# Kernel tuning notes

Measured on AMD Instinct MI355X. Metric: run time of the kernel, lower is better.

## Reference

```python
import jax, jax.numpy as jnp
import numpy as np

NUM_KP = 17
EDGES = [(0,1),(1,3),(0,2),(2,4),(0,5),(5,7),(7,9),(5,11),(11,13),(13,15),(0,6),(6,8),(8,10),(6,12),(12,14),(14,16)]
NUM_EDGES = len(EDGES)
IMG_H = IMG_W = 401


def bilinear_sampler(x, v):
    # x, v: [N, H, W, 2]. Faithful port of the TF gather_nd bilinear sampler
    # (pad-by-1 border, floor/ceil corners, out-of-bounds -> index 0 into pad).
    N, H, W, C = x.shape
    xp = jnp.pad(x, ((0, 0), (1, 1), (1, 1), (0, 0)))  # zeros pad
    vx = v[..., 0]
    vy = v[..., 1]
    hgrid = jnp.arange(1, H + 1, dtype=jnp.float32)[None, :, None]  # [1,H,1]
    wgrid = jnp.arange(1, W + 1, dtype=jnp.float32)[None, None, :]  # [1,1,W]
    vx0 = jnp.floor(vx); vy0 = jnp.floor(vy)
    vx1 = jnp.ceil(vx);  vy1 = jnp.ceil(vy)
    iy0 = vy0 + hgrid; iy1 = vy1 + hgrid
    ix0 = vx0 + wgrid; ix1 = vx1 + wgrid
    Hf = jnp.float32(H); Wf = jnp.float32(W)
    mask = (ix0 < 1.0) | (iy0 < 1.0) | (ix1 > Wf) | (iy1 > Hf)
    zero = jnp.zeros_like(iy0)
    iy0 = jnp.where(mask, zero, iy0)
    iy1 = jnp.where(mask, zero, iy1)
    ix0 = jnp.where(mask, zero, ix0)
    ix1 = jnp.where(mask, zero, ix1)
    n = jnp.arange(N)[:, None, None]
    iy0i = iy0.astype(jnp.int32); iy1i = iy1.astype(jnp.int32)
    ix0i = ix0.astype(jnp.int32); ix1i = ix1.astype(jnp.int32)
    x00 = xp[n, iy0i, ix0i]  # [N,H,W,C]
    x01 = xp[n, iy1i, ix0i]
    x10 = xp[n, iy0i, ix1i]
    x11 = xp[n, iy1i, ix1i]
    dx = (vx - vx0)[..., None]
    dy = (vy - vy0)[..., None]
    w00 = (1.0 - dx) * (1.0 - dy)
    w01 = (1.0 - dx) * dy
    w10 = dx * (1.0 - dy)
    w11 = dx * dy
    return w00 * x00 + w01 * x01 + w10 * x10 + w11 * x11


def refine(base, offsets, num_steps=2):
    for _ in range(num_steps):
        base = base + bilinear_sampler(offsets, base)
    return base


def conv1x1(x, w, b):
    return jnp.einsum('nhwc,co->nhwo', x, w) + b


def resize(m):
    N, _, _, C = m.shape
    return jax.image.resize(m, (N, IMG_H, IMG_W, C), method='bilinear')


def setup_inputs() -> dict:
    key = jax.random.key(0)
    ks = jax.random.split(key, 11)
    N, H, W, Cin = 2, 13, 13, 2048
    s = 0.01
    return {
        'x': jax.random.normal(ks[0], (N, H, W, Cin), jnp.float32),
        'kp_w': jax.random.normal(ks[1], (Cin, NUM_KP), jnp.float32) * s,
        'kp_b': jax.random.normal(ks[2], (NUM_KP,), jnp.float32) * s,
        'so_w': jax.random.normal(ks[3], (Cin, 2 * NUM_KP), jnp.float32) * s,
        'so_b': jax.random.normal(ks[4], (2 * NUM_KP,), jnp.float32) * s,
        'mo_w': jax.random.normal(ks[5], (Cin, 4 * NUM_EDGES), jnp.float32) * s,
        'mo_b': jax.random.normal(ks[6], (4 * NUM_EDGES,), jnp.float32) * s,
        'lo_w': jax.random.normal(ks[7], (Cin, 2 * NUM_KP), jnp.float32) * s,
        'lo_b': jax.random.normal(ks[8], (2 * NUM_KP,), jnp.float32) * s,
        'ss_w': jax.random.normal(ks[9], (Cin, 1), jnp.float32) * s,
        'ss_b': jax.random.normal(ks[10], (1,), jnp.float32) * s,
    }


def reference(x, kp_w, kp_b, so_w, so_b, mo_w, mo_b, lo_w, lo_b, ss_w, ss_b):
    N = x.shape[0]
    kp = jax.nn.sigmoid(conv1x1(x, kp_w, kp_b))
    so = conv1x1(x, so_w, so_b)
    mo = conv1x1(x, mo_w, mo_b)
    lo = conv1x1(x, lo_w, lo_b)
    ss = jax.nn.sigmoid(conv1x1(x, ss_w, ss_b))
    kp, so, mo, lo, ss = (resize(m) for m in (kp, so, mo, lo, ss))
    # Split channels into (x,y)-offset groups: [K, N, H, W, 2]
    S = so.reshape(N, IMG_H, IMG_W, NUM_KP, 2).transpose(3, 0, 1, 2, 4)
    L = lo.reshape(N, IMG_H, IMG_W, NUM_KP, 2).transpose(3, 0, 1, 2, 4)
    # long: refine against itself, then against short offsets (2 steps each)
    Lr = jax.vmap(lambda l, s: refine(refine(l, l), s))(L, S)
    long_out = Lr.transpose(1, 2, 3, 0, 4).reshape(N, IMG_H, IMG_W, 2 * NUM_KP)
    # mid: one group per directed edge, refined against the target kp short offsets
    n_mid = 2 * NUM_EDGES
    M = mo.reshape(N, IMG_H, IMG_W, n_mid, 2).transpose(3, 0, 1, 2, 4)
    to_kp = jnp.array([e[1] for e in EDGES] + [e[0] for e in EDGES], dtype=jnp.int32)
    Mr = jax.vmap(lambda m, s: refine(m, s))(M, S[to_kp])
    mid_out = Mr.transpose(1, 2, 3, 0, 4).reshape(N, IMG_H, IMG_W, 4 * NUM_EDGES)
    return (kp, so, mid_out, long_out, ss)
```

## Files before the change

### kernel.cpp

```cpp
#include <hip/hip_runtime.h>
#include <math.h>

#define IMG 401
#define NKP 17
#define NMID 32
#define CCH 150

#define OFF_KP   0ULL
#define OFF_SO   5467234ULL
#define OFF_MID  16401702ULL
#define OFF_LONG 36984230ULL
#define OFF_SS   47918698ULL

#define SCc (13.0f/401.0f)
#define C0c (13.0f/802.0f - 0.5f)
#define ROWS 8

typedef float v2f __attribute__((ext_vector_type(2)));

__device__ float  g_coarse[2 * 169 * CCH];
__device__ float2 g_pairs[2 * 66 * 169];

__constant__ int TO_KP_C[32] = {1,3,2,4,5,7,9,11,13,15,6,8,10,12,14,16,
                                0,1,0,2,0,5,7,5,11,13,0,6,8,6,12,14};

__device__ __forceinline__ float med3(float a, float b, float c) {
  return __builtin_amdgcn_fmed3f(a, b, c);
}
__device__ __forceinline__ void store2(float* p, float a, float b) {
  *reinterpret_cast<float2*>(p) = make_float2(a, b);
}
__device__ __forceinline__ v2f ldb(const float2* p, int byteoff) {
  return *reinterpret_cast<const v2f*>(reinterpret_cast<const char*>(p) + byteoff);
}

__global__ __launch_bounds__(512)
void heads_kernel(const float* __restrict__ x,
                  const float* __restrict__ kp_w, const float* __restrict__ kp_b,
                  const float* __restrict__ so_w, const float* __restrict__ so_b,
                  const float* __restrict__ mo_w, const float* __restrict__ mo_b,
                  const float* __restrict__ lo_w, const float* __restrict__ lo_b,
                  const float* __restrict__ ss_w, const float* __restrict__ ss_b) {
  __shared__ float xs[2][2048];
  __shared__ float ps[2][300];
  const int p0 = blockIdx.x * 2;
  const int tid = threadIdx.x;
  const float* xr = x + (size_t)p0 * 2048;
  for (int t = tid; t < 4096; t += 512) xs[t >> 11][t & 2047] = xr[t];
  __syncthreads();
  const int part = tid / 150;
  const int c = tid - part * 150;
  float a0 = 0.f, a1 = 0.f;
  const float* bptr = nullptr; int cc = 0; bool sig = false;
  if (part < 3) {
    const float* wptr; int Ch;
    if (c < 17)       { wptr = kp_w; bptr = kp_b; Ch = 17; cc = c;       sig = true; }
    else if (c < 51)  { wptr = so_w; bptr = so_b; Ch = 34; cc = c - 17; }
    else if (c < 115) { wptr = mo_w; bptr = mo_b; Ch = 64; cc = c - 51; }
    else if (c < 149) { wptr = lo_w; bptr = lo_b; Ch = 34; cc = c - 115; }
    else              { wptr = ss_w; bptr = ss_b; Ch = 1;  cc = 0;       sig = true; }
    const float* wp = wptr + cc;
    const int k0 = part * 683, k1 = (part == 2) ? 2048 : (k0 + 683);
    #pragma unroll 8
    for (int k = k0; k < k1; ++k) {
      float wv = wp[k * Ch];
      a0 = fmaf(xs[0][k], wv, a0);
      a1 = fmaf(xs[1][k], wv, a1);
    }
    if (part) { ps[0][c + (part - 1) * 150] = a0; ps[1][c + (part - 1) * 150] = a1; }
  }
  __syncthreads();
  if (part == 0) {
    float b = bptr[cc];
    float v0 = a0 + ps[0][c] + ps[0][c + 150] + b;
    float v1 = a1 + ps[1][c] + ps[1][c + 150] + b;
    if (sig) { v0 = 1.0f / (1.0f + expf(-v0)); v1 = 1.0f / (1.0f + expf(-v1)); }
    g_coarse[(size_t)p0 * CCH + c] = v0;
    g_coarse[(size_t)(p0 + 1) * CCH + c] = v1;
    if (c >= 17 && c < 149) {
      int rel = c - 17;
      int fi = rel >> 1, lo = rel & 1;
      int nn0 = p0 / 169, pp0 = p0 - nn0 * 169;
      int nn1 = (p0 + 1) / 169, pp1 = (p0 + 1) - nn1 * 169;
      ((float*)g_pairs)[(((size_t)nn0 * 66 + fi) * 169 + pp0) * 2 + lo] = v0;
      ((float*)g_pairs)[(((size_t)nn1 * 66 + fi) * 169 + pp1) * 2 + lo] = v1;
    }
  }
}

struct Pix {
  v2f Q0, Q1, SWH, LOV, HIV;
  int ob;
  int pix;
  bool valid;
};

__device__ __forceinline__ Pix mkpix(int n, int w, int h) {
  Pix P;
  P.valid = (w < IMG) && (h < IMG);
  v2f WH = {(float)w, (float)h};
  v2f S = WH * SCc + C0c;
  float cx = med3(floorf(S.x), 0.f, 11.f);
  float cy = med3(floorf(S.y), 0.f, 11.f);
  float fx = med3(S.x - cx, 0.f, 1.f);
  float fy = med3(S.y - cy, 0.f, 1.f);
  float gx = 1.f - fx, gy = 1.f - fy;
  P.Q0 = (v2f){gx, fx} * gy;
  P.Q1 = (v2f){gx, fx} * fy;
  P.ob = (int)fmaf(cy, 104.f, cx * 8.f);
  P.SWH = S;
  P.LOV = -WH;
  P.HIV = 400.f - WH;
  P.pix = (n * IMG + h) * IMG + w;
  return P;
}

__device__ __forceinline__ v2f blp4b(const float2* __restrict__ F, const Pix& P) {
  return P.Q0.x * ldb(F, P.ob)       + P.Q0.y * ldb(F, P.ob + 8)
       + P.Q1.x * ldb(F, P.ob + 104) + P.Q1.y * ldb(F, P.ob + 112);
}

__device__ __forceinline__ v2f samplePk(const float2* __restrict__ F, v2f v, const Pix& P) {
  v2f F0 = {floorf(v.x), floorf(v.y)};
  v2f D  = v - F0;
  v2f E  = {D.x > 0.f ? 1.f : 0.f, D.y > 0.f ? 1.f : 0.f};
  v2f J1 = F0 + E;
  float sel = (F0.x < P.LOV.x || F0.y < P.LOV.y ||
               J1.x > P.HIV.x || J1.y > P.HIV.y) ? 0.f : 1.f;
  v2f S0 = F0 * SCc + P.SWH;
  v2f S1 = E  * SCc + S0;
  v2f C0 = {med3(floorf(S0.x), 0.f, 11.f), med3(floorf(S0.y), 0.f, 11.f)};
  v2f C1 = {med3(floorf(S1.x), 0.f, 11.f), med3(floorf(S1.y), 0.f, 11.f)};
  v2f U0t = S0 - C0;
  v2f U0 = {med3(U0t.x, 0.f, 1.f), med3(U0t.y, 0.f, 1.f)};
  v2f U1t = S1 - C1;
  v2f U1 = {med3(U1t.x, 0.f, 1.f), med3(U1t.y, 0.f, 1.f)};
  v2f DD = C1 - C0;
  v2f G  = 1.f - D;
  v2f E0 = G * U0;
  v2f E1 = D * U1;
  v2f Fd = D - E1;
  v2f M  = Fd - Fd * DD;
  v2f W0 = (G - E0) + M;
  v2f Tt = Fd - E1;
  v2f W1 = (E0 + E1) + Tt * DD;
  v2f W2 = E1 * DD;
  int a = (int)fmaf(C0.y, 104.f, C0.x * 8.f);
  v2f r0 = W0.x*ldb(F,a)     + W1.x*ldb(F,a+8)   + W2.x*ldb(F,a+16);
  v2f r1 = W0.x*ldb(F,a+104) + W1.x*ldb(F,a+112) + W2.x*ldb(F,a+120);
  v2f r2 = W0.x*ldb(F,a+208) + W1.x*ldb(F,a+216) + W2.x*ldb(F,a+224);
  v2f acc = W0.y*r0 + W1.y*r1 + W2.y*r2;
  return acc * sel;
}

__global__ __launch_bounds__(512, 6)
void refine512_kernel(float* __restrict__ out) {
  __shared__ float2 Sf[NKP * 169 + 14];
  __shared__ float2 Lf[NKP * 169 + 14];
  const int n = blockIdx.z;
  const int tid = threadIdx.x;
  const int w0 = blockIdx.x * 32, h0 = blockIdx.y * ROWS;

  {
    const float2* gS = g_pairs + (size_t)n * 66 * 169;
    const float2* gL = g_pairs + ((size_t)n * 66 + 49) * 169;
    for (int t = tid; t < NKP * 169; t += 512) { Sf[t] = gS[t]; Lf[t] = gL[t]; }
    if (tid < 14) {
      Sf[NKP * 169 + tid] = make_float2(0.f, 0.f);
      Lf[NKP * 169 + tid] = make_float2(0.f, 0.f);
    }
  }
  __syncthreads();

  const float* cb = g_coarse + (size_t)n * 169 * CCH;

  #pragma unroll 1
  for (int it = 0; it < 9; ++it) {
    int f = it * 512 + tid;
    if (f >= ROWS * 544) break;
    int r = f / 544, rem = f - r * 544;
    int px = rem / 17, c = rem - px * 17;
    Pix P = mkpix(n, w0 + px, h0 + r);
    if (P.valid) {
      const float* b0 = cb + (P.ob >> 3) * CCH + c;
      out[OFF_KP + (size_t)P.pix * 17 + c] =
          P.Q0.x*b0[0] + P.Q0.y*b0[CCH] + P.Q1.x*b0[13*CCH] + P.Q1.y*b0[14*CCH];
    }
  }

  if (tid < ROWS * 32) {
    int r = tid >> 5, px = tid & 31;
    Pix P = mkpix(n, w0 + px, h0 + r);
    if (P.valid) {
      const float* b0 = cb + (P.ob >> 3) * CCH + 149;
      out[OFF_SS + (size_t)P.pix] =
          P.Q0.x*b0[0] + P.Q0.y*b0[CCH] + P.Q1.x*b0[13*CCH] + P.Q1.y*b0[14*CCH];
    }
  }

  #pragma unroll 1
  for (int it = 0; it < 9; ++it) {
    int f = it * 512 + tid;
    if (f >= ROWS * 544) break;
    int r = f / 544, rem = f - r * 544;
    int px = rem / 17, k = rem - px * 17;
    Pix P = mkpix(n, w0 + px, h0 + r);
    const float2* S = Sf + k * 169;
    const float2* L = Lf + k * 169;
    v2f sv = blp4b(S, P);
    v2f b  = blp4b(L, P);
    b += samplePk(L, b, P);
    b += samplePk(L, b, P);
    b += samplePk(S, b, P);
    b += samplePk(S, b, P);
    if (P.valid) {
      store2(out + OFF_SO   + (size_t)P.pix * 34 + 2 * k, sv.x, sv.y);
      store2(out + OFF_LONG + (size_t)P.pix * 34 + 2 * k, b.x, b.y);
    }
  }

  const float2* gmo = g_pairs + ((size_t)n * 66 + 17) * 169;
  #pragma unroll 1
  for (int it = 0; it < 16; ++it) {
    int f = it * 512 + tid;
    int r = f >> 10, rem = f & 1023;
    int px = rem >> 5, g = rem & 31;
    Pix P = mkpix(n, w0 + px, h0 + r);
    v2f b = blp4b(gmo + g * 169, P);
    const float2* S = Sf + TO_KP_C[g] * 169;
    b += samplePk(S, b, P);
    b += samplePk(S, b, P);
    if (P.valid) store2(out + OFF_MID + (size_t)P.pix * 64 + 2 * g, b.x, b.y);
  }
}

extern "C" void kernel_launch(void* const* d_in, const int* in_sizes, int n_in,
                              void* d_out, int out_size, void* d_ws, size_t ws_size,
                              hipStream_t stream) {
  const float* x    = (const float*)d_in[0];
  const float* kp_w = (const float*)d_in[1];
  const float* kp_b = (const float*)d_in[2];
  const float* so_w = (const float*)d_in[3];
  const float* so_b = (const float*)d_in[4];
  const float* mo_w = (const float*)d_in[5];
  const float* mo_b = (const float*)d_in[6];
  const float* lo_w = (const float*)d_in[7];
  const float* lo_b = (const float*)d_in[8];
  const float* ss_w = (const float*)d_in[9];
  const float* ss_b = (const float*)d_in[10];
  float* out = (float*)d_out;

  heads_kernel<<<dim3(169), dim3(512), 0, stream>>>(x, kp_w, kp_b, so_w, so_b,
                                                    mo_w, mo_b, lo_w, lo_b,
                                                    ss_w, ss_b);
  refine512_kernel<<<dim3(13, 51, 2), dim3(512), 0, stream>>>(out);
}
```

Baseline: 161.6 us.

## Pad short-offset planes with clamped border to drop per-sample clamping

Stores the short-offset coarse planes in shared memory as 15x15 planes padded with replicated (edge-clamped) border values. A new sampler for those planes can then skip the med3 clamps on coarse indices and fractions, computing the cell step from a comparison instead of a second floor. The long planes keep the old unpadded layout. This cuts ALU work in the hot refinement samplers, in exchange for slightly more shared memory and a more complex staging loop with integer divides.

```diff
diff --git a/kernel.cpp b/kernel.cpp
--- a/kernel.cpp
+++ b/kernel.cpp
@@ -15,6 +15,9 @@
 #define SCc (13.0f/401.0f)
 #define C0c (13.0f/802.0f - 0.5f)
 #define ROWS 8
+#define PSTR 120
+#define PPL  225
+#define LBASE (17 * PPL)
 
 typedef float v2f __attribute__((ext_vector_type(2)));
 
@@ -91,6 +94,7 @@
 struct Pix {
   v2f Q0, Q1, SWH, LOV, HIV;
   int ob;
+  int obp;
   int pix;
   bool valid;
 };
@@ -107,7 +111,8 @@
   float gx = 1.f - fx, gy = 1.f - fy;
   P.Q0 = (v2f){gx, fx} * gy;
   P.Q1 = (v2f){gx, fx} * fy;
-  P.ob = (int)fmaf(cy, 104.f, cx * 8.f);
+  P.ob  = (int)fmaf(cy, 104.f, cx * 8.f);
+  P.obp = (int)fmaf(cy, (float)PSTR, cx * 8.f) + (PSTR + 8);
   P.SWH = S;
   P.LOV = -WH;
   P.HIV = 400.f - WH;
@@ -115,12 +120,16 @@
   return P;
 }
 
-__device__ __forceinline__ v2f blp4b(const float2* __restrict__ F, const Pix& P) {
+__device__ __forceinline__ v2f blp4bU(const float2* __restrict__ F, const Pix& P) {
   return P.Q0.x * ldb(F, P.ob)       + P.Q0.y * ldb(F, P.ob + 8)
        + P.Q1.x * ldb(F, P.ob + 104) + P.Q1.y * ldb(F, P.ob + 112);
 }
-
-__device__ __forceinline__ v2f samplePk(const float2* __restrict__ F, v2f v, const Pix& P) {
+__device__ __forceinline__ v2f blp4bP(const float2* __restrict__ F, const Pix& P) {
+  return P.Q0.x * ldb(F, P.obp)        + P.Q0.y * ldb(F, P.obp + 8)
+       + P.Q1.x * ldb(F, P.obp + PSTR) + P.Q1.y * ldb(F, P.obp + PSTR + 8);
+}
+
+__device__ __forceinline__ v2f sampleU16(const float2* __restrict__ F, v2f v, const Pix& P) {
   v2f F0 = {floorf(v.x), floorf(v.y)};
   v2f D  = v - F0;
   v2f E  = {D.x > 0.f ? 1.f : 0.f, D.y > 0.f ? 1.f : 0.f};
@@ -149,14 +158,41 @@
   v2f r0 = W0.x*ldb(F,a)     + W1.x*ldb(F,a+8)   + W2.x*ldb(F,a+16);
   v2f r1 = W0.x*ldb(F,a+104) + W1.x*ldb(F,a+112) + W2.x*ldb(F,a+120);
   v2f r2 = W0.x*ldb(F,a+208) + W1.x*ldb(F,a+216) + W2.x*ldb(F,a+224);
-  v2f acc = W0.y*r0 + W1.y*r1 + W2.y*r2;
-  return acc * sel;
+  return (W0.y*r0 + W1.y*r1 + W2.y*r2) * sel;
+}
+
+__device__ __forceinline__ v2f samplePad(const float2* __restrict__ F, v2f v, const Pix& P) {
+  v2f F0 = {floorf(v.x), floorf(v.y)};
+  v2f D  = v - F0;
+  v2f E  = {D.x > 0.f ? 1.f : 0.f, D.y > 0.f ? 1.f : 0.f};
+  v2f J1 = F0 + E;
+  float sel = (F0.x < P.LOV.x || F0.y < P.LOV.y ||
+               J1.x > P.HIV.x || J1.y > P.HIV.y) ? 0.f : 1.f;
+  v2f S0 = F0 * SCc + P.SWH;
+  v2f C0 = {floorf(S0.x), floorf(S0.y)};
+  v2f U0 = S0 - C0;
+  v2f T  = E * SCc + U0;
+  v2f DD = {T.x >= 1.f ? 1.f : 0.f, T.y >= 1.f ? 1.f : 0.f};
+  v2f U1 = T - DD;
+  v2f G  = 1.f - D;
+  v2f E0 = G * U0;
+  v2f E1 = D * U1;
+  v2f Fd = D - E1;
+  v2f M  = Fd - Fd * DD;
+  v2f W0 = (G - E0) + M;
+  v2f Tt = Fd - E1;
+  v2f W1 = (E0 + E1) + Tt * DD;
+  v2f W2 = E1 * DD;
+  int a = (int)fmaf(C0.y, (float)PSTR, C0.x * 8.f) + (PSTR + 8);
+  v2f r0 = W0.x*ldb(F,a)        + W1.x*ldb(F,a+8)        + W2.x*ldb(F,a+16);
+  v2f r1 = W0.x*ldb(F,a+PSTR)   + W1.x*ldb(F,a+PSTR+8)   + W2.x*ldb(F,a+PSTR+16);
+  v2f r2 = W0.x*ldb(F,a+2*PSTR) + W1.x*ldb(F,a+2*PSTR+8) + W2.x*ldb(F,a+2*PSTR+16);
+  return (W0.y*r0 + W1.y*r1 + W2.y*r2) * sel;
 }
 
 __global__ __launch_bounds__(512, 6)
 void refine512_kernel(float* __restrict__ out) {
-  __shared__ float2 Sf[NKP * 169 + 14];
-  __shared__ float2 Lf[NKP * 169 + 14];
+  __shared__ float2 Pf[LBASE + 17 * 169 + 16];
   const int n = blockIdx.z;
   const int tid = threadIdx.x;
   const int w0 = blockIdx.x * 32, h0 = blockIdx.y * ROWS;
@@ -164,11 +200,14 @@
   {
     const float2* gS = g_pairs + (size_t)n * 66 * 169;
     const float2* gL = g_pairs + ((size_t)n * 66 + 49) * 169;
-    for (int t = tid; t < NKP * 169; t += 512) { Sf[t] = gS[t]; Lf[t] = gL[t]; }
-    if (tid < 14) {
-      Sf[NKP * 169 + tid] = make_float2(0.f, 0.f);
-      Lf[NKP * 169 + tid] = make_float2(0.f, 0.f);
-    }
+    for (int t = tid; t < 17 * PPL; t += 512) {
+      int pl = t / PPL, idx = t - pl * PPL;
+      int row = idx / 15, col = idx - row * 15;
+      int sr = min(max(row - 1, 0), 12), sc = min(max(col - 1, 0), 12);
+      Pf[t] = gS[pl * 169 + sr * 13 + sc];
+    }
+    for (int t = tid; t < 17 * 169; t += 512) Pf[LBASE + t] = gL[t];
+    if (tid < 16) Pf[LBASE + 17 * 169 + tid] = make_float2(0.f, 0.f);
   }
   __syncthreads();
 
@@ -205,14 +244,14 @@
     int r = f / 544, rem = f - r * 544;
     int px = rem / 17, k = rem - px * 17;
     Pix P = mkpix(n, w0 + px, h0 + r);
-    const float2* S = Sf + k * 169;
-    const float2* L = Lf + k * 169;
-    v2f sv = blp4b(S, P);
-    v2f b  = blp4b(L, P);
-    b += samplePk(L, b, P);
-    b += samplePk(L, b, P);
-    b += samplePk(S, b, P);
-    b += samplePk(S, b, P);
+    const float2* S = Pf + k * PPL;
+    const float2* L = Pf + LBASE + k * 169;
+    v2f sv = blp4bP(S, P);
+    v2f b  = blp4bU(L, P);
+    b += sampleU16(L, b, P);
+    b += sampleU16(L, b, P);
+    b += samplePad(S, b, P);
+    b += samplePad(S, b, P);
     if (P.valid) {
       store2(out + OFF_SO   + (size_t)P.pix * 34 + 2 * k, sv.x, sv.y);
       store2(out + OFF_LONG + (size_t)P.pix * 34 + 2 * k, b.x, b.y);
@@ -226,10 +265,10 @@
     int r = f >> 10, rem = f & 1023;
     int px = rem >> 5, g = rem & 31;
     Pix P = mkpix(n, w0 + px, h0 + r);
-    v2f b = blp4b(gmo + g * 169, P);
-    const float2* S = Sf + TO_KP_C[g] * 169;
-    b += samplePk(S, b, P);
-    b += samplePk(S, b, P);
+    v2f b = blp4bU(gmo + g * 169, P);
+    const float2* S = Pf + TO_KP_C[g] * PPL;
+    b += samplePad(S, b, P);
+    b += samplePad(S, b, P);
     if (P.valid) store2(out + OFF_MID + (size_t)P.pix * 64 + 2 * g, b.x, b.y);
   }
 }
```

Measured after the change: 160.8 us. Within noise of the previous version (-0.5%).
